# Performance work log

Measured on AMD Instinct MI355X. Metric: run time of the kernel, lower is better.

## Reference

```python
import jax, jax.numpy as jnp
import numpy as np

N = 50000      # nodes
T = 24         # sequence length
D_IN = 16      # lstm input dim
H = 64         # lstm hidden dim
SD = 9         # static feature dim
G_IN, G_HID, G_OUT = 64, 64, 1
E = 1600000    # edges
NUM_GRAPHS = 500


def setup_inputs() -> dict:
    key = jax.random.key(0)
    ks = jax.random.split(key, 16)
    s = 0.1
    return {
        "x": jax.random.normal(ks[0], (N, T, D_IN), dtype=jnp.float32),
        "sdi": jax.random.normal(ks[1], (N, SD), dtype=jnp.float32),
        "edge_index": jax.random.randint(ks[2], (2, E), 0, N, dtype=jnp.int64),
        "batch": jnp.sort(jax.random.randint(ks[3], (N,), 0, NUM_GRAPHS, dtype=jnp.int64)),
        # LSTM params (torch gate order: i, f, g, o)
        "W_ih": s * jax.random.normal(ks[4], (4 * H, D_IN), dtype=jnp.float32),
        "W_hh": s * jax.random.normal(ks[5], (4 * H, H), dtype=jnp.float32),
        "b_ih": s * jax.random.normal(ks[6], (4 * H,), dtype=jnp.float32),
        "b_hh": s * jax.random.normal(ks[7], (4 * H,), dtype=jnp.float32),
        # Linear l1: (hidden + static) -> graph_input
        "l1_W": s * jax.random.normal(ks[8], (G_IN, H + SD), dtype=jnp.float32),
        "l1_b": s * jax.random.normal(ks[9], (G_IN,), dtype=jnp.float32),
        # GCNConv layers (weight stored [out, in] like torch Linear)
        "gcn1_W": s * jax.random.normal(ks[10], (G_HID, G_IN), dtype=jnp.float32),
        "gcn1_b": s * jax.random.normal(ks[11], (G_HID,), dtype=jnp.float32),
        "gcn2_W": s * jax.random.normal(ks[12], (G_OUT, G_HID), dtype=jnp.float32),
        "gcn2_b": s * jax.random.normal(ks[13], (G_OUT,), dtype=jnp.float32),
    }


def _lstm_last_hidden(x, W_ih, W_hh, b_ih, b_hh):
    # x: [N, T, D]; returns final hidden state h_T: [N, H]
    xg = jnp.einsum("ntd,gd->tng", x, W_ih) + (b_ih + b_hh)  # [T, N, 4H]
    h0 = jnp.zeros((x.shape[0], H), x.dtype)
    c0 = jnp.zeros((x.shape[0], H), x.dtype)

    def step(carry, g_t):
        h, c = carry
        g = g_t + h @ W_hh.T
        i, f, gg, o = jnp.split(g, 4, axis=-1)
        i = jax.nn.sigmoid(i)
        f = jax.nn.sigmoid(f)
        gg = jnp.tanh(gg)
        o = jax.nn.sigmoid(o)
        c = f * c + i * gg
        h = o * jnp.tanh(c)
        return (h, c), None

    (h, _), _ = jax.lax.scan(step, (h0, c0), xg)
    return h


def _gcn_conv(x, edge_index, W, b):
    # PyG GCNConv: add self-loops, symmetric normalization, scatter-add at dst.
    n = x.shape[0]
    loop = jnp.arange(n, dtype=edge_index.dtype)
    row = jnp.concatenate([edge_index[0], loop])  # src
    col = jnp.concatenate([edge_index[1], loop])  # dst
    deg = jax.ops.segment_sum(jnp.ones_like(col, dtype=x.dtype), col, num_segments=n)
    dis = jnp.where(deg > 0, jax.lax.rsqrt(jnp.maximum(deg, 1.0)), 0.0)
    norm = dis[row] * dis[col]                    # [E + N]
    h = x @ W.T                                   # [N, out]
    msg = h[row] * norm[:, None]                  # gather + scale
    out = jax.ops.segment_sum(msg, col, num_segments=n)
    return out + b


def reference(x, sdi, edge_index, batch, W_ih, W_hh, b_ih, b_hh,
              l1_W, l1_b, gcn1_W, gcn1_b, gcn2_W, gcn2_b):
    h = _lstm_last_hidden(x, W_ih, W_hh, b_ih, b_hh)       # [N, H]
    z = jnp.concatenate([h, sdi], axis=-1) @ l1_W.T + l1_b  # [N, G_IN]
    z = jax.nn.relu(_gcn_conv(z, edge_index, gcn1_W, gcn1_b))
    z = _gcn_conv(z, edge_index, gcn2_W, gcn2_b)            # [N, 1]
    # global mean pool over graph ids
    sums = jax.ops.segment_sum(z, batch, num_segments=NUM_GRAPHS)
    cnts = jax.ops.segment_sum(jnp.ones((z.shape[0],), z.dtype), batch, num_segments=NUM_GRAPHS)
    pooled = sums / jnp.maximum(cnts, 1.0)[:, None]         # [G, 1]
    return pooled.reshape(-1)
```

## Files before the change

kernel.cpp:

```cpp
#include <hip/hip_runtime.h>
#include <hip/hip_bf16.h>

#define N_NODES 50000
#define T_SEQ 24
#define D_IN 16
#define H_DIM 64
#define SD 9
#define E_EDGES 1600000
#define NUM_GRAPHS 500
#define NBLK 196
#define LSTM_BLOCKS 3125

typedef _Float16 half8 __attribute__((ext_vector_type(8)));
typedef _Float16 half4 __attribute__((ext_vector_type(4)));
typedef float floatx4 __attribute__((ext_vector_type(4)));

__device__ __forceinline__ float fsig(float x) {
    return __fdividef(1.0f, 1.0f + __expf(-x));
}
__device__ __forceinline__ float ftanh(float x) {
    return 1.0f - __fdividef(2.0f, 1.0f + __expf(2.0f * x));
}

__global__ __launch_bounds__(256, 2) void lstm_mfma(
    const float* __restrict__ x,
    const float* __restrict__ W_ih, const float* __restrict__ W_hh,
    const float* __restrict__ b_ih, const float* __restrict__ b_hh,
    const float* __restrict__ Wc, const float* __restrict__ bc,
    const float* __restrict__ sdi,
    const int* __restrict__ ei, int* __restrict__ cnt,
    _Float16* __restrict__ m_out)
{
    __shared__ _Float16 smem[2048 + 24 * 16 * 16];
    _Float16* hb0 = smem;
    _Float16* hb1 = smem + 1024;
    _Float16* xbuf = smem + 2048;

    const int tid  = threadIdx.x;
    const int lane = tid & 63;
    const int w    = tid >> 6;
    const int lr   = lane & 15;
    const int lg   = lane >> 4;
    const int nbase = blockIdx.x * 16;

    for (int e = blockIdx.x * 256 + tid; e < E_EDGES; e += LSTM_BLOCKS * 256) {
        const int c = ei[E_EDGES + e];
        if ((unsigned)c < N_NODES) atomicAdd(&cnt[c], 1);
    }

    half8 bw[4][3];
    float bias[4];
#pragma unroll
    for (int ct = 0; ct < 4; ct++) {
        const int r = ct * 64 + w * 16 + lr;
        bias[ct] = b_ih[r] + b_hh[r];
#pragma unroll
        for (int kt = 0; kt < 2; kt++) {
            const float* p = W_hh + r * 64 + kt * 32 + 8 * lg;
            half8 f;
#pragma unroll
            for (int e = 0; e < 8; e++) f[e] = (_Float16)p[e];
            bw[ct][kt] = f;
        }
        half8 f = {(_Float16)0, (_Float16)0, (_Float16)0, (_Float16)0,
                   (_Float16)0, (_Float16)0, (_Float16)0, (_Float16)0};
        if (lg < 2) {
            const float* p = W_ih + r * 16 + 8 * lg;
#pragma unroll
            for (int e = 0; e < 8; e++) f[e] = (_Float16)p[e];
        }
        bw[ct][2] = f;
    }

    half8 bwc[3];
    {
        const int fr = w * 16 + lr;
#pragma unroll
        for (int kt = 0; kt < 2; kt++) {
            const float* p = Wc + fr * 73 + kt * 32 + 8 * lg;
            half8 f;
#pragma unroll
            for (int e = 0; e < 8; e++) f[e] = (_Float16)p[e];
            bwc[kt] = f;
        }
        half8 f = {(_Float16)0, (_Float16)0, (_Float16)0, (_Float16)0,
                   (_Float16)0, (_Float16)0, (_Float16)0, (_Float16)0};
#pragma unroll
        for (int e = 0; e < 8; e++) {
            const int k2 = 8 * lg + e;
            if (k2 < 9) f[e] = (_Float16)Wc[fr * 73 + 64 + k2];
            else if (k2 == 9) f[e] = (_Float16)bc[fr];
        }
        bwc[2] = f;
    }

#pragma unroll
    for (int it = 0; it < 6; it++) {
        const int f4 = tid + it * 256;
        const int fi = f4 * 4;
        const int n  = fi / 384;
        const int rem = fi - n * 384;
        const int t  = rem >> 4;
        const int d  = rem & 15;
        const float4 v = *reinterpret_cast<const float4*>(
            x + (size_t)(nbase + n) * 384 + rem);
        half4 hv = {(_Float16)v.x, (_Float16)v.y, (_Float16)v.z, (_Float16)v.w};
        *reinterpret_cast<half4*>(&xbuf[t * 256 + n * 16 + d]) = hv;
    }
    if (tid < 128) { ((int*)hb0)[tid] = 0; ((int*)hb0)[tid + 128] = 0; ((int*)hb0)[tid + 256] = 0; ((int*)hb0)[tid + 384] = 0; }

    const int u = w * 16 + lr;
    int ra[2];
#pragma unroll
    for (int kt = 0; kt < 2; kt++)
        ra[kt] = lr * 64 + 8 * ((4 * kt + lg) ^ (lr & 7));
    int woff[4];
#pragma unroll
    for (int j = 0; j < 4; j++) {
        const int nj = 4 * lg + j;
        woff[j] = nj * 64 + (u & 7) + 8 * ((u >> 3) ^ (nj & 7));
    }
    const int xro = lr * 16 + 8 * (lg & 1);

    float c_reg[4];
#pragma unroll
    for (int j = 0; j < 4; j++) c_reg[j] = 0.0f;

    __syncthreads();

    auto step = [&](int tl, _Float16* hR, _Float16* hW) {
        floatx4 acc[4];
#pragma unroll
        for (int ct = 0; ct < 4; ct++) {
            floatx4 a = {bias[ct], bias[ct], bias[ct], bias[ct]};
            acc[ct] = a;
        }
        const half8 ax = *reinterpret_cast<const half8*>(&xbuf[tl * 256 + xro]);
        const half8 ah0 = *reinterpret_cast<const half8*>(&hR[ra[0]]);
        const half8 ah1 = *reinterpret_cast<const half8*>(&hR[ra[1]]);
#pragma unroll
        for (int ct = 0; ct < 4; ct++)
            acc[ct] = __builtin_amdgcn_mfma_f32_16x16x32_f16(ah0, bw[ct][0], acc[ct], 0, 0, 0);
#pragma unroll
        for (int ct = 0; ct < 4; ct++)
            acc[ct] = __builtin_amdgcn_mfma_f32_16x16x32_f16(ah1, bw[ct][1], acc[ct], 0, 0, 0);
#pragma unroll
        for (int ct = 0; ct < 4; ct++)
            acc[ct] = __builtin_amdgcn_mfma_f32_16x16x32_f16(ax, bw[ct][2], acc[ct], 0, 0, 0);

#pragma unroll
        for (int j = 0; j < 4; j++) {
            const float ig = fsig(acc[0][j]);
            const float fg = fsig(acc[1][j]);
            const float gg = ftanh(acc[2][j]);
            const float og = fsig(acc[3][j]);
            const float cv = fg * c_reg[j] + ig * gg;
            c_reg[j] = cv;
            const float hv = og * ftanh(cv);
            hW[woff[j]] = (_Float16)hv;
        }
        __syncthreads();
    };

    for (int tb = 0; tb < 6; tb++) {
        const int t0 = tb * 4;
        step(t0 + 0, hb0, hb1);
        step(t0 + 1, hb1, hb0);
        step(t0 + 2, hb0, hb1);
        step(t0 + 3, hb1, hb0);
    }

    half8 axs = {(_Float16)0, (_Float16)0, (_Float16)0, (_Float16)0,
                 (_Float16)0, (_Float16)0, (_Float16)0, (_Float16)0};
#pragma unroll
    for (int e = 0; e < 8; e++) {
        const int k2 = 8 * lg + e;
        if (k2 < 9) axs[e] = (_Float16)sdi[(size_t)(nbase + lr) * SD + k2];
        else if (k2 == 9) axs[e] = (_Float16)1.0f;
    }
    const half8 fh0 = *reinterpret_cast<const half8*>(&hb0[ra[0]]);
    const half8 fh1 = *reinterpret_cast<const half8*>(&hb0[ra[1]]);
    floatx4 am = {0.0f, 0.0f, 0.0f, 0.0f};
    am = __builtin_amdgcn_mfma_f32_16x16x32_f16(fh0, bwc[0], am, 0, 0, 0);
    am = __builtin_amdgcn_mfma_f32_16x16x32_f16(fh1, bwc[1], am, 0, 0, 0);
    am = __builtin_amdgcn_mfma_f32_16x16x32_f16(axs, bwc[2], am, 0, 0, 0);
#pragma unroll
    for (int j = 0; j < 4; j++) {
        const int gn = nbase + 4 * lg + j;
        m_out[(size_t)gn * 64 + u] = (_Float16)am[j];
    }
}

__global__ __launch_bounds__(256) void scanA(const int* __restrict__ cnt,
                                             int* __restrict__ ptr,
                                             float* __restrict__ dis,
                                             int* __restrict__ bsum)
{
    __shared__ int wsum[4];
    const int tid = threadIdx.x, lane = tid & 63, wv = tid >> 6;
    const int i = blockIdx.x * 256 + tid;
    const int orig = (i < N_NODES) ? cnt[i] : 0;
    int v = orig;
#pragma unroll
    for (int d = 1; d < 64; d <<= 1) {
        int nb = __shfl_up(v, d, 64);
        if (lane >= d) v += nb;
    }
    if (lane == 63) wsum[wv] = v;
    __syncthreads();
    int woff = 0;
#pragma unroll
    for (int k = 0; k < 3; k++) if (k < wv) woff += wsum[k];
    if (i < N_NODES) {
        ptr[i] = woff + v - orig;
        dis[i] = rsqrtf((float)(orig + 1));
    }
    if (tid == 255) bsum[blockIdx.x] = woff + v;
}

__global__ __launch_bounds__(256) void scanB(const int* __restrict__ bsum,
                                             int* __restrict__ boff,
                                             int* __restrict__ ptr,
                                             float* __restrict__ gzero)
{
    __shared__ int wsum[4];
    const int tid = threadIdx.x, lane = tid & 63, wv = tid >> 6;
#pragma unroll
    for (int k = 0; k < 4; k++) gzero[tid + k * 256] = 0.0f;
    const int orig = (tid < NBLK) ? bsum[tid] : 0;
    int v = orig;
#pragma unroll
    for (int d = 1; d < 64; d <<= 1) {
        int nb = __shfl_up(v, d, 64);
        if (lane >= d) v += nb;
    }
    if (lane == 63) wsum[wv] = v;
    __syncthreads();
    int woff = 0;
#pragma unroll
    for (int k = 0; k < 3; k++) if (k < wv) woff += wsum[k];
    if (tid < NBLK) boff[tid] = woff + v - orig;
    if (tid == 255) ptr[N_NODES] = woff + v;
}

__global__ __launch_bounds__(256) void scanC(int* __restrict__ ptr,
                                             const int* __restrict__ boff,
                                             int* __restrict__ cursor)
{
    const int i = blockIdx.x * 256 + threadIdx.x;
    if (i < N_NODES) {
        const int p = ptr[i] + boff[blockIdx.x];
        ptr[i] = p;
        cursor[i] = p;
    }
}

__global__ void fill_csr(const int* __restrict__ ei, int* __restrict__ cursor,
                         int* __restrict__ csr)
{
    int e = blockIdx.x * 256 + threadIdx.x;
    if (e < E_EDGES) {
        int r = ei[e];
        int c = ei[E_EDGES + e];
        if ((unsigned)r < N_NODES && (unsigned)c < N_NODES) {
            int slot = atomicAdd(&cursor[c], 1);
            csr[slot] = r;
        }
    }
}

__global__ void combine_w(const float* __restrict__ g1W, const float* __restrict__ l1W,
                          const float* __restrict__ l1b,
                          float* __restrict__ Wc, float* __restrict__ bc)
{
    int idx = blockIdx.x * 256 + threadIdx.x;
    int o = idx / 74, j = idx - o * 74;
    if (o >= 64) return;
    float acc = 0.0f;
    if (j < 73) {
#pragma unroll 8
        for (int k = 0; k < 64; k++) acc += g1W[o * 64 + k] * l1W[k * 73 + j];
        Wc[o * 73 + j] = acc;
    } else {
#pragma unroll 8
        for (int k = 0; k < 64; k++) acc += g1W[o * 64 + k] * l1b[k];
        bc[o] = acc;
    }
}

__global__ __launch_bounds__(256) void gatherfin1s2(
    const int* __restrict__ ptr, const int* __restrict__ csr,
    const _Float16* __restrict__ m, const float* __restrict__ dis,
    const float* __restrict__ b1, const float* __restrict__ W2,
    float* __restrict__ s2)
{
    const int wid = (blockIdx.x * 256 + threadIdx.x) >> 6;
    const int f = threadIdx.x & 63;
    if (wid >= N_NODES) return;
    const int b = ptr[wid];
    const int e = ptr[wid + 1];
    float a0 = 0.0f, a1 = 0.0f, a2 = 0.0f, a3 = 0.0f;
    float a4 = 0.0f, a5 = 0.0f, a6 = 0.0f, a7 = 0.0f;
    int i = b;
    for (; i + 8 <= e; i += 8) {
        const int s0 = csr[i],     s1 = csr[i + 1], s2i = csr[i + 2], s3 = csr[i + 3];
        const int s4 = csr[i + 4], s5 = csr[i + 5], s6 = csr[i + 6], s7 = csr[i + 7];
        a0 += dis[s0] * (float)m[(size_t)s0 * 64 + f];
        a1 += dis[s1] * (float)m[(size_t)s1 * 64 + f];
        a2 += dis[s2i] * (float)m[(size_t)s2i * 64 + f];
        a3 += dis[s3] * (float)m[(size_t)s3 * 64 + f];
        a4 += dis[s4] * (float)m[(size_t)s4 * 64 + f];
        a5 += dis[s5] * (float)m[(size_t)s5 * 64 + f];
        a6 += dis[s6] * (float)m[(size_t)s6 * 64 + f];
        a7 += dis[s7] * (float)m[(size_t)s7 * 64 + f];
    }
    for (; i < e; i++) { const int s = csr[i]; a0 += dis[s] * (float)m[(size_t)s * 64 + f]; }
    const float dn = dis[wid];
    const float self = dn * (float)m[(size_t)wid * 64 + f];
    const float v = dn * ((((a0 + a1) + (a2 + a3)) + ((a4 + a5) + (a6 + a7))) + self) + b1[f];
    const float z1 = v > 0.0f ? v : 0.0f;
    float p = z1 * W2[f];
#pragma unroll
    for (int off = 32; off >= 1; off >>= 1) p += __shfl_xor(p, off, 64);
    if (f == 0) s2[wid] = dn * p;
}

__global__ void gather2fin(const int* __restrict__ ptr, const int* __restrict__ csr,
                           const float* __restrict__ s2, const float* __restrict__ dis,
                           const float* __restrict__ b2, const int* __restrict__ batch,
                           float* __restrict__ gsum, float* __restrict__ gcnt)
{
    int n = blockIdx.x * 256 + threadIdx.x;
    if (n >= N_NODES) return;
    const int b = ptr[n];
    const int e = ptr[n + 1];
    float a0 = 0.0f, a1 = 0.0f, a2 = 0.0f, a3 = 0.0f;
    float a4 = 0.0f, a5 = 0.0f, a6 = 0.0f, a7 = 0.0f;
    int i = b;
    for (; i + 8 <= e; i += 8) {
        a0 += s2[csr[i]];
        a1 += s2[csr[i + 1]];
        a2 += s2[csr[i + 2]];
        a3 += s2[csr[i + 3]];
        a4 += s2[csr[i + 4]];
        a5 += s2[csr[i + 5]];
        a6 += s2[csr[i + 6]];
        a7 += s2[csr[i + 7]];
    }
    for (; i < e; i++) a0 += s2[csr[i]];
    const float z2 = dis[n] * ((((a0 + a1) + (a2 + a3)) + ((a4 + a5) + (a6 + a7))) + s2[n]) + b2[0];
    const int g = batch[n];
    if ((unsigned)g < NUM_GRAPHS) {
        atomicAdd(&gsum[g], z2);
        atomicAdd(&gcnt[g], 1.0f);
    }
}

__global__ void pooldiv(const float* __restrict__ gsum, const float* __restrict__ gcnt,
                        float* __restrict__ out)
{
    int g = blockIdx.x * 256 + threadIdx.x;
    if (g < NUM_GRAPHS) out[g] = gsum[g] / fmaxf(gcnt[g], 1.0f);
}

extern "C" void kernel_launch(void* const* d_in, const int* in_sizes, int n_in,
                              void* d_out, int out_size, void* d_ws, size_t ws_size,
                              hipStream_t stream)
{
    const float* x     = (const float*)d_in[0];
    const float* sdi   = (const float*)d_in[1];
    const int*   ei    = (const int*)d_in[2];
    const int*   batch = (const int*)d_in[3];
    const float* W_ih  = (const float*)d_in[4];
    const float* W_hh  = (const float*)d_in[5];
    const float* b_ih  = (const float*)d_in[6];
    const float* b_hh  = (const float*)d_in[7];
    const float* l1_W  = (const float*)d_in[8];
    const float* l1_b  = (const float*)d_in[9];
    const float* g1_W  = (const float*)d_in[10];
    const float* g1_b  = (const float*)d_in[11];
    const float* g2_W  = (const float*)d_in[12];
    const float* g2_b  = (const float*)d_in[13];
    float* out = (float*)d_out;

    float* ws   = (float*)d_ws;
    _Float16* C16 = (_Float16*)(ws + 6400000);
    float* dis  = ws + 9600000;
    float* s2   = dis + 50000;
    float* gsum = s2 + 50000;
    float* gcnt = gsum + 500;
    int* cnt    = (int*)(gsum + 1024);
    int* ptr    = cnt + 50000;
    int* cursor = ptr + 50001;
    int* csr    = cursor + 50000;
    float* Wc   = (float*)(csr + E_EDGES);
    float* bc   = Wc + 64 * 73;
    int* bsum   = (int*)(bc + 64);
    int* boff   = bsum + NBLK;

    const int featBlocks = (N_NODES * 64 + 255) / 256;
    const int edgeBlocks = (E_EDGES + 255) / 256;

    hipMemsetAsync(cnt, 0, 50000 * sizeof(int), stream);
    combine_w<<<(64 * 74 + 255) / 256, 256, 0, stream>>>(g1_W, l1_W, l1_b, Wc, bc);

    lstm_mfma<<<LSTM_BLOCKS, 256, 0, stream>>>(x, W_ih, W_hh, b_ih, b_hh,
                                               Wc, bc, sdi, ei, cnt, C16);

    scanA<<<NBLK, 256, 0, stream>>>(cnt, ptr, dis, bsum);
    scanB<<<1, 256, 0, stream>>>(bsum, boff, ptr, gsum);
    scanC<<<NBLK, 256, 0, stream>>>(ptr, boff, cursor);
    fill_csr<<<edgeBlocks, 256, 0, stream>>>(ei, cursor, csr);

    gatherfin1s2<<<featBlocks, 256, 0, stream>>>(ptr, csr, C16, dis, g1_b, g2_W, s2);

    gather2fin<<<NBLK, 256, 0, stream>>>(ptr, csr, s2, dis, g2_b, batch, gsum, gcnt);
    pooldiv<<<2, 256, 0, stream>>>(gsum, gcnt, out);
}
```

Measured before the change: 485.3 us.

## Split GCN gathers across more waves per node to raise parallelism

```diff
diff --git a/kernel.cpp b/kernel.cpp
--- a/kernel.cpp
+++ b/kernel.cpp
@@ -294,65 +294,58 @@
     const float* __restrict__ b1, const float* __restrict__ W2,
     float* __restrict__ s2)
 {
-    const int wid = (blockIdx.x * 256 + threadIdx.x) >> 6;
+    __shared__ float part[4][64];
+    const int dst = blockIdx.x;
     const int f = threadIdx.x & 63;
-    if (wid >= N_NODES) return;
-    const int b = ptr[wid];
-    const int e = ptr[wid + 1];
-    float a0 = 0.0f, a1 = 0.0f, a2 = 0.0f, a3 = 0.0f;
-    float a4 = 0.0f, a5 = 0.0f, a6 = 0.0f, a7 = 0.0f;
-    int i = b;
-    for (; i + 8 <= e; i += 8) {
-        const int s0 = csr[i],     s1 = csr[i + 1], s2i = csr[i + 2], s3 = csr[i + 3];
-        const int s4 = csr[i + 4], s5 = csr[i + 5], s6 = csr[i + 6], s7 = csr[i + 7];
+    const int wv = threadIdx.x >> 6;
+    const int b = ptr[dst];
+    const int e = ptr[dst + 1];
+    float a0 = 0.0f, a1 = 0.0f;
+    int i = b + wv;
+    for (; i + 4 < e; i += 8) {
+        const int s0 = csr[i];
+        const int s1 = csr[i + 4];
         a0 += dis[s0] * (float)m[(size_t)s0 * 64 + f];
         a1 += dis[s1] * (float)m[(size_t)s1 * 64 + f];
-        a2 += dis[s2i] * (float)m[(size_t)s2i * 64 + f];
-        a3 += dis[s3] * (float)m[(size_t)s3 * 64 + f];
-        a4 += dis[s4] * (float)m[(size_t)s4 * 64 + f];
-        a5 += dis[s5] * (float)m[(size_t)s5 * 64 + f];
-        a6 += dis[s6] * (float)m[(size_t)s6 * 64 + f];
-        a7 += dis[s7] * (float)m[(size_t)s7 * 64 + f];
-    }
-    for (; i < e; i++) { const int s = csr[i]; a0 += dis[s] * (float)m[(size_t)s * 64 + f]; }
-    const float dn = dis[wid];
-    const float self = dn * (float)m[(size_t)wid * 64 + f];
-    const float v = dn * ((((a0 + a1) + (a2 + a3)) + ((a4 + a5) + (a6 + a7))) + self) + b1[f];
-    const float z1 = v > 0.0f ? v : 0.0f;
-    float p = z1 * W2[f];
-#pragma unroll
-    for (int off = 32; off >= 1; off >>= 1) p += __shfl_xor(p, off, 64);
-    if (f == 0) s2[wid] = dn * p;
-}
-
-__global__ void gather2fin(const int* __restrict__ ptr, const int* __restrict__ csr,
-                           const float* __restrict__ s2, const float* __restrict__ dis,
-                           const float* __restrict__ b2, const int* __restrict__ batch,
-                           float* __restrict__ gsum, float* __restrict__ gcnt)
-{
-    int n = blockIdx.x * 256 + threadIdx.x;
+    }
+    if (i < e) { const int s = csr[i]; a0 += dis[s] * (float)m[(size_t)s * 64 + f]; }
+    part[wv][f] = a0 + a1;
+    __syncthreads();
+    if (wv == 0) {
+        const float dn = dis[dst];
+        const float self = dn * (float)m[(size_t)dst * 64 + f];
+        const float sum = (part[0][f] + part[1][f]) + (part[2][f] + part[3][f]);
+        const float v = dn * (sum + self) + b1[f];
+        const float z1 = v > 0.0f ? v : 0.0f;
+        float p = z1 * W2[f];
+#pragma unroll
+        for (int off = 32; off >= 1; off >>= 1) p += __shfl_xor(p, off, 64);
+        if (f == 0) s2[dst] = dn * p;
+    }
+}
+
+__global__ __launch_bounds__(256) void gather2fin(
+    const int* __restrict__ ptr, const int* __restrict__ csr,
+    const float* __restrict__ s2, const float* __restrict__ dis,
+    const float* __restrict__ b2, const int* __restrict__ batch,
+    float* __restrict__ gsum, float* __restrict__ gcnt)
+{
+    const int n = (blockIdx.x * 256 + threadIdx.x) >> 6;
+    const int lane = threadIdx.x & 63;
     if (n >= N_NODES) return;
     const int b = ptr[n];
     const int e = ptr[n + 1];
-    float a0 = 0.0f, a1 = 0.0f, a2 = 0.0f, a3 = 0.0f;
-    float a4 = 0.0f, a5 = 0.0f, a6 = 0.0f, a7 = 0.0f;
-    int i = b;
-    for (; i + 8 <= e; i += 8) {
-        a0 += s2[csr[i]];
-        a1 += s2[csr[i + 1]];
-        a2 += s2[csr[i + 2]];
-        a3 += s2[csr[i + 3]];
-        a4 += s2[csr[i + 4]];
-        a5 += s2[csr[i + 5]];
-        a6 += s2[csr[i + 6]];
-        a7 += s2[csr[i + 7]];
-    }
-    for (; i < e; i++) a0 += s2[csr[i]];
-    const float z2 = dis[n] * ((((a0 + a1) + (a2 + a3)) + ((a4 + a5) + (a6 + a7))) + s2[n]) + b2[0];
-    const int g = batch[n];
-    if ((unsigned)g < NUM_GRAPHS) {
-        atomicAdd(&gsum[g], z2);
-        atomicAdd(&gcnt[g], 1.0f);
+    float a = 0.0f;
+    for (int i = b + lane; i < e; i += 64) a += s2[csr[i]];
+#pragma unroll
+    for (int off = 32; off >= 1; off >>= 1) a += __shfl_xor(a, off, 64);
+    if (lane == 0) {
+        const float z2 = dis[n] * (a + s2[n]) + b2[0];
+        const int g = batch[n];
+        if ((unsigned)g < NUM_GRAPHS) {
+            atomicAdd(&gsum[g], z2);
+            atomicAdd(&gcnt[g], 1.0f);
+        }
     }
 }
 
@@ -398,7 +391,6 @@
     int* bsum   = (int*)(bc + 64);
     int* boff   = bsum + NBLK;
 
-    const int featBlocks = (N_NODES * 64 + 255) / 256;
     const int edgeBlocks = (E_EDGES + 255) / 256;
 
     hipMemsetAsync(cnt, 0, 50000 * sizeof(int), stream);
@@ -412,8 +404,8 @@
     scanC<<<NBLK, 256, 0, stream>>>(ptr, boff, cursor);
     fill_csr<<<edgeBlocks, 256, 0, stream>>>(ei, cursor, csr);
 
-    gatherfin1s2<<<featBlocks, 256, 0, stream>>>(ptr, csr, C16, dis, g1_b, g2_W, s2);
-
-    gather2fin<<<NBLK, 256, 0, stream>>>(ptr, csr, s2, dis, g2_b, batch, gsum, gcnt);
+    gatherfin1s2<<<N_NODES, 256, 0, stream>>>(ptr, csr, C16, dis, g1_b, g2_W, s2);
+
+    gather2fin<<<(N_NODES + 3) / 4, 256, 0, stream>>>(ptr, csr, s2, dis, g2_b, batch, gsum, gcnt);
     pooldiv<<<2, 256, 0, stream>>>(gsum, gcnt, out);
 }
```

Measured after the change: 607.8 us. 25.2% more time.
